# Kernel tuning notes

Measured on AMD Instinct MI355X. Metric: run time of the kernel, lower is better.

The kernel has to match this reference:

```python
import jax, jax.numpy as jnp
import numpy as np

B, H, S, D = 4, 16, 2048, 64

def setup_inputs() -> dict:
    key = jax.random.key(0)
    kq, kk, kv = jax.random.split(key, 3)
    q = jax.random.normal(kq, (B, H, S, D), dtype=jnp.float32)
    k = jax.random.normal(kk, (B, H, S, D), dtype=jnp.float32)
    v = jax.random.normal(kv, (B, H, S, D), dtype=jnp.float32)
    return {"q_tensor": q, "k_tensor": k, "v_tensor": v}

def reference(q_tensor, k_tensor, v_tensor):
    # scores: [B, H, S, S]
    inv_scale = 1.0 / jnp.sqrt(jnp.float32(k_tensor.shape[-1]))
    scores = jnp.einsum('bhqd,bhkd->bhqk', q_tensor, k_tensor) * inv_scale
    attn = jax.nn.softmax(scores, axis=-1)
    # dropout p=0.0 -> identity
    out = jnp.einsum('bhqk,bhkd->bhqd', attn, v_tensor)
    return out
```

## Files before the change

### kernel.cpp

```cpp
#include <hip/hip_runtime.h>
#include <hip/hip_bf16.h>

#define S_LEN 2048
#define D_DIM 64
#define BH 64
#define NWARP 4
#define QW 32
#define QBLK (NWARP * QW)
#define KVBLK 64
#define NKT (S_LEN / KVBLK)
#define NWG (BH * S_LEN / QBLK)
#define TILE_ELEMS (KVBLK * D_DIM)
#define TILE_BYTES (TILE_ELEMS * 2)

typedef __bf16 bf16_t;
typedef bf16_t bf16x8 __attribute__((ext_vector_type(8)));
typedef float f32x4 __attribute__((ext_vector_type(4)));
typedef float f32x16 __attribute__((ext_vector_type(16)));

typedef const __attribute__((address_space(1))) void gvoid_t;
typedef __attribute__((address_space(3))) void lvoid_t;

__device__ __forceinline__ int swz64(int row, int col) {
  return (row << 6) + (col ^ ((row & 7) << 3));
}

union W4 { unsigned u[4]; bf16x8 v; };
union PK { bf16_t h[2]; unsigned u; };

__global__ __launch_bounds__(256)
void preconv(const float* __restrict__ K, const float* __restrict__ V,
             bf16_t* __restrict__ Kws, bf16_t* __restrict__ Vws) {
  const int tile = blockIdx.x;
  const int bh = tile >> 5, kt = tile & 31;
  const size_t base = (size_t)bh * S_LEN * D_DIM + (size_t)kt * KVBLK * D_DIM;
  const int tid = threadIdx.x;
  bf16_t* ko = Kws + (size_t)tile * TILE_ELEMS;
  bf16_t* vo = Vws + (size_t)tile * TILE_ELEMS;

  const int krow = tid >> 2, kcb = tid & 3;
  const float* ks = K + base + (size_t)krow * D_DIM + kcb * 16;
  f32x4 kr[4];
#pragma unroll
  for (int i = 0; i < 4; ++i) kr[i] = *(const f32x4*)(ks + i * 4);
#pragma unroll
  for (int half = 0; half < 2; ++half) {
    bf16x8 f;
#pragma unroll
    for (int j = 0; j < 4; ++j) {
      f[j]     = (bf16_t)kr[half * 2][j];
      f[4 + j] = (bf16_t)kr[half * 2 + 1][j];
    }
    *(bf16x8*)&ko[swz64(krow, kcb * 16 + half * 8)] = f;
  }

  const int vkp = tid & 31, vdb = tid >> 5;
  const int vk0 = vkp * 2;
  const int vcol = (((vk0 >> 2) ^ (vk0 >> 3)) & 1) ? (vk0 ^ 12) : vk0;
  const float* vs = V + base + (size_t)vk0 * D_DIM + vdb * 8;
  f32x4 vr[4];
  vr[0] = *(const f32x4*)vs;           vr[1] = *(const f32x4*)(vs + 4);
  vr[2] = *(const f32x4*)(vs + D_DIM); vr[3] = *(const f32x4*)(vs + D_DIM + 4);
#pragma unroll
  for (int j = 0; j < 8; ++j) {
    PK p;
    p.h[0] = (bf16_t)((j < 4) ? vr[0][j] : vr[1][j - 4]);
    p.h[1] = (bf16_t)((j < 4) ? vr[2][j] : vr[3][j - 4]);
    *(unsigned*)&vo[swz64(vdb * 8 + j, vcol)] = p.u;
  }
}

__global__ __launch_bounds__(256, 3)
void sdpa_fwd_ws(const float* __restrict__ Q, const bf16_t* __restrict__ Kws,
                 const bf16_t* __restrict__ Vws, float* __restrict__ O) {
  __shared__ bf16_t Klds[2][TILE_ELEMS];
  __shared__ bf16_t VTlds[2][TILE_ELEMS];

  const int bid = blockIdx.x;
  const int lb  = (bid & 7) * (NWG / 8) + (bid >> 3);
  const int bx  = lb & 15;
  const int bh  = lb >> 4;

  const int tid  = threadIdx.x;
  const int wave = tid >> 6;
  const int lane = tid & 63;
  const int lq   = lane & 31;
  const int h    = lane >> 5;

  const size_t base = (size_t)bh * S_LEN * D_DIM;
  const int q0 = bx * QBLK + wave * QW;
  const float qscale = 0.125f * 1.44269504089f;

  bf16x8 qf[4];
  {
    const float* qp = Q + base + (size_t)(q0 + lq) * D_DIM + h * 8;
#pragma unroll
    for (int c = 0; c < 4; ++c) {
      f32x4 a = *(const f32x4*)(qp + c * 16);
      f32x4 b = *(const f32x4*)(qp + c * 16 + 4);
      bf16x8 f;
#pragma unroll
      for (int j = 0; j < 4; ++j) {
        f[j]     = (bf16_t)(a[j] * qscale);
        f[4 + j] = (bf16_t)(b[j] * qscale);
      }
      qf[c] = f;
    }
  }

  bf16x8 ones;
#pragma unroll
  for (int j = 0; j < 8; ++j) ones[j] = (bf16_t)1.0f;

  const char* kg = (const char*)(Kws + (size_t)(bh * NKT) * TILE_ELEMS)
                   + wave * 2048 + lane * 16;
  const char* vg = (const char*)(Vws + (size_t)(bh * NKT) * TILE_ELEMS)
                   + wave * 2048 + lane * 16;

  auto issue = [&](int kt, int buf) {
    const char* ksrc = kg + (size_t)kt * TILE_BYTES;
    const char* vsrc = vg + (size_t)kt * TILE_BYTES;
    char* kd = (char*)&Klds[buf][0] + wave * 2048;
    char* vd = (char*)&VTlds[buf][0] + wave * 2048;
    __builtin_amdgcn_global_load_lds((gvoid_t*)ksrc,          (lvoid_t*)kd,          16, 0, 0);
    __builtin_amdgcn_global_load_lds((gvoid_t*)(ksrc + 1024), (lvoid_t*)(kd + 1024), 16, 0, 0);
    __builtin_amdgcn_global_load_lds((gvoid_t*)vsrc,          (lvoid_t*)vd,          16, 0, 0);
    __builtin_amdgcn_global_load_lds((gvoid_t*)(vsrc + 1024), (lvoid_t*)(vd + 1024), 16, 0, 0);
  };

  f32x16 acc0 = {}, acc1 = {};
  f32x16 accl = {};

  issue(0, 0);

  int cur = 0;
  for (int kt = 0; kt < NKT; ++kt) {
    __builtin_amdgcn_s_barrier();
    if (kt + 1 < NKT) {
      issue(kt + 1, cur ^ 1);
      asm volatile("s_waitcnt vmcnt(4)" ::: "memory");
    } else {
      asm volatile("s_waitcnt vmcnt(0)" ::: "memory");
    }
    __builtin_amdgcn_s_barrier();
    __builtin_amdgcn_sched_barrier(0);

    const bf16_t* Kb = Klds[cur];
    const bf16_t* Vb = VTlds[cur];

    f32x16 st0 = {}, st1 = {};
    __builtin_amdgcn_s_setprio(1);
#pragma unroll
    for (int c = 0; c < 4; ++c) {
      bf16x8 kf0 = *(const bf16x8*)&Kb[swz64(lq, c * 16 + h * 8)];
      bf16x8 kf1 = *(const bf16x8*)&Kb[swz64(32 + lq, c * 16 + h * 8)];
      st0 = __builtin_amdgcn_mfma_f32_32x32x16_bf16(kf0, qf[c], st0, 0, 0, 0);
      st1 = __builtin_amdgcn_mfma_f32_32x32x16_bf16(kf1, qf[c], st1, 0, 0, 0);
    }
    __builtin_amdgcn_s_setprio(0);

#pragma unroll
    for (int r = 0; r < 16; ++r) {
      st0[r] = exp2f(st0[r]);
      st1[r] = exp2f(st1[r]);
    }

    bf16x8 pf[4];
#pragma unroll
    for (int s2 = 0; s2 < 2; ++s2) {
      W4 w0, w1;
#pragma unroll
      for (int i = 0; i < 4; ++i) {
        PK a, b;
        a.h[0] = (bf16_t)(s2 ? st1[2 * i]     : st0[2 * i]);
        a.h[1] = (bf16_t)(s2 ? st1[2 * i + 1] : st0[2 * i + 1]);
        b.h[0] = (bf16_t)(s2 ? st1[8 + 2 * i]     : st0[8 + 2 * i]);
        b.h[1] = (bf16_t)(s2 ? st1[8 + 2 * i + 1] : st0[8 + 2 * i + 1]);
        w0.u[i] = a.u; w1.u[i] = b.u;
      }
      pf[s2 * 2] = w0.v; pf[s2 * 2 + 1] = w1.v;
    }

    __builtin_amdgcn_s_setprio(1);
#pragma unroll
    for (int kc = 0; kc < 4; ++kc) {
      bf16x8 vf0 = *(const bf16x8*)&Vb[swz64(lq, kc * 16 + h * 8)];
      bf16x8 vf1 = *(const bf16x8*)&Vb[swz64(32 + lq, kc * 16 + h * 8)];
      acc0 = __builtin_amdgcn_mfma_f32_32x32x16_bf16(vf0, pf[kc], acc0, 0, 0, 0);
      acc1 = __builtin_amdgcn_mfma_f32_32x32x16_bf16(vf1, pf[kc], acc1, 0, 0, 0);
      accl = __builtin_amdgcn_mfma_f32_32x32x16_bf16(ones, pf[kc], accl, 0, 0, 0);
    }
    __builtin_amdgcn_s_setprio(0);

    cur ^= 1;
  }

  float invl = 1.0f / accl[0];
  float* op = O + base + (size_t)(q0 + lq) * D_DIM;
#pragma unroll
  for (int r = 0; r < 16; ++r) {
    int d = (r & 3) + 8 * (r >> 2) + 4 * h;
    op[d]      = acc0[r] * invl;
    op[32 + d] = acc1[r] * invl;
  }
}

__global__ __launch_bounds__(256, 2)
void sdpa_fwd_fb(const float* __restrict__ Q, const float* __restrict__ K,
                 const float* __restrict__ V, float* __restrict__ O) {
  __shared__ bf16_t Klds[2][KVBLK * D_DIM];
  __shared__ bf16_t VTlds[2][D_DIM * KVBLK];

  const int bid = blockIdx.x;
  const int lb  = (bid & 7) * (NWG / 8) + (bid >> 3);
  const int bx  = lb & 15;
  const int bh  = lb >> 4;

  const int tid  = threadIdx.x;
  const int wave = tid >> 6;
  const int lane = tid & 63;
  const int lq   = lane & 31;
  const int h    = lane >> 5;

  const size_t base = (size_t)bh * S_LEN * D_DIM;
  const int q0 = bx * QBLK + wave * QW;
  const float qscale = 0.125f * 1.44269504089f;

  bf16x8 qf[4];
  {
    const float* qp = Q + base + (size_t)(q0 + lq) * D_DIM + h * 8;
#pragma unroll
    for (int c = 0; c < 4; ++c) {
      f32x4 a = *(const f32x4*)(qp + c * 16);
      f32x4 b = *(const f32x4*)(qp + c * 16 + 4);
      bf16x8 f;
#pragma unroll
      for (int j = 0; j < 4; ++j) {
        f[j]     = (bf16_t)(a[j] * qscale);
        f[4 + j] = (bf16_t)(b[j] * qscale);
      }
      qf[c] = f;
    }
  }

  const int krow = tid >> 2, kcb = tid & 3;
  const int vkp = tid & 31, vdb = tid >> 5;
  const int vk0 = vkp * 2;
  const int vcol = (((vk0 >> 2) ^ (vk0 >> 3)) & 1) ? (vk0 ^ 12) : vk0;

  f32x4 kr[4], vr[4];

  auto issue = [&](int kt) {
    const float* ks = K + base + (size_t)(kt * KVBLK + krow) * D_DIM + kcb * 16;
#pragma unroll
    for (int i = 0; i < 4; ++i) kr[i] = *(const f32x4*)(ks + i * 4);
    const float* vs = V + base + (size_t)(kt * KVBLK + vk0) * D_DIM + vdb * 8;
    vr[0] = *(const f32x4*)vs;           vr[1] = *(const f32x4*)(vs + 4);
    vr[2] = *(const f32x4*)(vs + D_DIM); vr[3] = *(const f32x4*)(vs + D_DIM + 4);
  };

  auto stage = [&](int buf) {
#pragma unroll
    for (int half = 0; half < 2; ++half) {
      bf16x8 f;
#pragma unroll
      for (int j = 0; j < 4; ++j) {
        f[j]     = (bf16_t)kr[half * 2][j];
        f[4 + j] = (bf16_t)kr[half * 2 + 1][j];
      }
      *(bf16x8*)&Klds[buf][swz64(krow, kcb * 16 + half * 8)] = f;
    }
#pragma unroll
    for (int j = 0; j < 8; ++j) {
      PK p;
      p.h[0] = (bf16_t)((j < 4) ? vr[0][j] : vr[1][j - 4]);
      p.h[1] = (bf16_t)((j < 4) ? vr[2][j] : vr[3][j - 4]);
      *(unsigned*)&VTlds[buf][swz64(vdb * 8 + j, vcol)] = p.u;
    }
  };

  f32x16 acc0 = {}, acc1 = {};
  float m = -1e30f, l = 0.f;

  issue(0);
  stage(0);
  __syncthreads();

  for (int kt = 0; kt < NKT; ++kt) {
    const int cur = kt & 1;
    if (kt + 1 < NKT) issue(kt + 1);

    const bf16_t* Kb = Klds[cur];
    const bf16_t* Vb = VTlds[cur];

    f32x16 st0 = {}, st1 = {};
    __builtin_amdgcn_s_setprio(1);
#pragma unroll
    for (int c = 0; c < 4; ++c) {
      bf16x8 kf0 = *(const bf16x8*)&Kb[swz64(lq, c * 16 + h * 8)];
      bf16x8 kf1 = *(const bf16x8*)&Kb[swz64(32 + lq, c * 16 + h * 8)];
      st0 = __builtin_amdgcn_mfma_f32_32x32x16_bf16(kf0, qf[c], st0, 0, 0, 0);
      st1 = __builtin_amdgcn_mfma_f32_32x32x16_bf16(kf1, qf[c], st1, 0, 0, 0);
    }
    __builtin_amdgcn_s_setprio(0);

    float t16[16];
#pragma unroll
    for (int r = 0; r < 16; ++r) t16[r] = fmaxf(st0[r], st1[r]);
#pragma unroll
    for (int off = 8; off > 0; off >>= 1)
#pragma unroll
      for (int i = 0; i < off; ++i) t16[i] = fmaxf(t16[i], t16[i + off]);
    float pmax = fmaxf(t16[0], __shfl_xor(t16[0], 32, 64));

    if (!__all(pmax - m <= 8.0f)) {
      float mn = fmaxf(m, pmax);
      float al = exp2f(m - mn);
      m = mn; l *= al;
#pragma unroll
      for (int r = 0; r < 16; ++r) { acc0[r] *= al; acc1[r] *= al; }
    }

#pragma unroll
    for (int r = 0; r < 16; ++r) {
      st0[r] = exp2f(st0[r] - m);
      st1[r] = exp2f(st1[r] - m);
    }
    float sm[16];
#pragma unroll
    for (int r = 0; r < 16; ++r) sm[r] = st0[r] + st1[r];
#pragma unroll
    for (int off = 8; off > 0; off >>= 1)
#pragma unroll
      for (int i = 0; i < off; ++i) sm[i] += sm[i + off];
    l += sm[0] + __shfl_xor(sm[0], 32, 64);

    bf16x8 pf[4];
#pragma unroll
    for (int s2 = 0; s2 < 2; ++s2) {
      W4 w0, w1;
#pragma unroll
      for (int i = 0; i < 4; ++i) {
        PK a, b;
        a.h[0] = (bf16_t)(s2 ? st1[2 * i]     : st0[2 * i]);
        a.h[1] = (bf16_t)(s2 ? st1[2 * i + 1] : st0[2 * i + 1]);
        b.h[0] = (bf16_t)(s2 ? st1[8 + 2 * i]     : st0[8 + 2 * i]);
        b.h[1] = (bf16_t)(s2 ? st1[8 + 2 * i + 1] : st0[8 + 2 * i + 1]);
        w0.u[i] = a.u; w1.u[i] = b.u;
      }
      pf[s2 * 2] = w0.v; pf[s2 * 2 + 1] = w1.v;
    }

    __builtin_amdgcn_s_setprio(1);
#pragma unroll
    for (int kc = 0; kc < 4; ++kc) {
      bf16x8 vf0 = *(const bf16x8*)&Vb[swz64(lq, kc * 16 + h * 8)];
      bf16x8 vf1 = *(const bf16x8*)&Vb[swz64(32 + lq, kc * 16 + h * 8)];
      acc0 = __builtin_amdgcn_mfma_f32_32x32x16_bf16(vf0, pf[kc], acc0, 0, 0, 0);
      acc1 = __builtin_amdgcn_mfma_f32_32x32x16_bf16(vf1, pf[kc], acc1, 0, 0, 0);
    }
    __builtin_amdgcn_s_setprio(0);

    if (kt + 1 < NKT) stage(cur ^ 1);
    __syncthreads();
  }

  float invl = 1.0f / l;
  float* op = O + base + (size_t)(q0 + lq) * D_DIM;
#pragma unroll
  for (int r = 0; r < 16; ++r) {
    int d = (r & 3) + 8 * (r >> 2) + 4 * h;
    op[d]      = acc0[r] * invl;
    op[32 + d] = acc1[r] * invl;
  }
}

extern "C" void kernel_launch(void* const* d_in, const int* in_sizes, int n_in,
                              void* d_out, int out_size, void* d_ws, size_t ws_size,
                              hipStream_t stream) {
  const float* q = (const float*)d_in[0];
  const float* k = (const float*)d_in[1];
  const float* v = (const float*)d_in[2];
  float* o = (float*)d_out;

  const size_t tile_cnt = (size_t)BH * NKT;
  const size_t need = 2 * tile_cnt * TILE_ELEMS * sizeof(bf16_t);

  if (ws_size >= need) {
    bf16_t* kws = (bf16_t*)d_ws;
    bf16_t* vws = kws + tile_cnt * TILE_ELEMS;
    preconv<<<(int)tile_cnt, 256, 0, stream>>>(k, v, kws, vws);
    sdpa_fwd_ws<<<NWG, 256, 0, stream>>>(q, kws, vws, o);
  } else {
    sdpa_fwd_fb<<<NWG, 256, 0, stream>>>(q, k, v, o);
  }
}
```

Measured before the change: 123.0 us.

## Software-pipeline QK of next tile with softmax/PV of current tile

Restructures the main fast-path loop so each tile's QK^T MFMAs are issued before the previous tile's exp/PV stage, unrolled by two over even/odd LDS buffers with a single full wait-and-barrier per tile. The row sum is now taken with a VALU reduction plus a lane shuffle instead of an extra MFMA against a ones vector, and exp2f becomes the raw hardware builtin. This is meant to overlap matrix-core work with the exponentials and cut one MFMA per kv chunk, at the cost of more live registers and a stricter vmcnt(0) wait before each barrier.

```diff
diff --git a/kernel.cpp b/kernel.cpp
--- a/kernel.cpp
+++ b/kernel.cpp
@@ -108,10 +108,6 @@
     }
   }
 
-  bf16x8 ones;
-#pragma unroll
-  for (int j = 0; j < 8; ++j) ones[j] = (bf16_t)1.0f;
-
   const char* kg = (const char*)(Kws + (size_t)(bh * NKT) * TILE_ELEMS)
                    + wave * 2048 + lane * 16;
   const char* vg = (const char*)(Vws + (size_t)(bh * NKT) * TILE_ELEMS)
@@ -129,21 +125,188 @@
   };
 
   f32x16 acc0 = {}, acc1 = {};
-  f32x16 accl = {};
+  float l = 0.f;
+
+  auto qk = [&](const bf16_t* Kb, f32x16& s0, f32x16& s1) {
+    f32x16 z = {};
+    s0 = z; s1 = z;
+    __builtin_amdgcn_s_setprio(1);
+#pragma unroll
+    for (int c = 0; c < 4; ++c) {
+      bf16x8 kf0 = *(const bf16x8*)&Kb[swz64(lq, c * 16 + h * 8)];
+      bf16x8 kf1 = *(const bf16x8*)&Kb[swz64(32 + lq, c * 16 + h * 8)];
+      s0 = __builtin_amdgcn_mfma_f32_32x32x16_bf16(kf0, qf[c], s0, 0, 0, 0);
+      s1 = __builtin_amdgcn_mfma_f32_32x32x16_bf16(kf1, qf[c], s1, 0, 0, 0);
+    }
+    __builtin_amdgcn_s_setprio(0);
+  };
+
+  auto finish = [&](const bf16_t* Vb, f32x16& s0, f32x16& s1) {
+#pragma unroll
+    for (int r = 0; r < 16; ++r) {
+      s0[r] = __builtin_amdgcn_exp2f(s0[r]);
+      s1[r] = __builtin_amdgcn_exp2f(s1[r]);
+    }
+    float sm[16];
+#pragma unroll
+    for (int r = 0; r < 16; ++r) sm[r] = s0[r] + s1[r];
+#pragma unroll
+    for (int off = 8; off > 0; off >>= 1)
+#pragma unroll
+      for (int i = 0; i < off; ++i) sm[i] += sm[i + off];
+    l += sm[0] + __shfl_xor(sm[0], 32, 64);
+
+    bf16x8 pf[4];
+#pragma unroll
+    for (int s2 = 0; s2 < 2; ++s2) {
+      W4 w0, w1;
+#pragma unroll
+      for (int i = 0; i < 4; ++i) {
+        PK a, b;
+        a.h[0] = (bf16_t)(s2 ? s1[2 * i]     : s0[2 * i]);
+        a.h[1] = (bf16_t)(s2 ? s1[2 * i + 1] : s0[2 * i + 1]);
+        b.h[0] = (bf16_t)(s2 ? s1[8 + 2 * i]     : s0[8 + 2 * i]);
+        b.h[1] = (bf16_t)(s2 ? s1[8 + 2 * i + 1] : s0[8 + 2 * i + 1]);
+        w0.u[i] = a.u; w1.u[i] = b.u;
+      }
+      pf[s2 * 2] = w0.v; pf[s2 * 2 + 1] = w1.v;
+    }
+
+    __builtin_amdgcn_s_setprio(1);
+#pragma unroll
+    for (int kc = 0; kc < 4; ++kc) {
+      bf16x8 vf0 = *(const bf16x8*)&Vb[swz64(lq, kc * 16 + h * 8)];
+      bf16x8 vf1 = *(const bf16x8*)&Vb[swz64(32 + lq, kc * 16 + h * 8)];
+      acc0 = __builtin_amdgcn_mfma_f32_32x32x16_bf16(vf0, pf[kc], acc0, 0, 0, 0);
+      acc1 = __builtin_amdgcn_mfma_f32_32x32x16_bf16(vf1, pf[kc], acc1, 0, 0, 0);
+    }
+    __builtin_amdgcn_s_setprio(0);
+  };
+
+#define WAITBAR() do { \
+    asm volatile("s_waitcnt vmcnt(0) lgkmcnt(0)" ::: "memory"); \
+    __builtin_amdgcn_s_barrier(); \
+  } while (0)
+
+  f32x16 stE0, stE1, stO0, stO1;
 
   issue(0, 0);
-
-  int cur = 0;
+  WAITBAR();
+  issue(1, 1);
+  qk(Klds[0], stE0, stE1);
+
+#pragma unroll 1
+  for (int t = 1; t < NKT; t += 2) {
+    finish(VTlds[0], stE0, stE1);
+    WAITBAR();
+    if (t + 1 < NKT) issue(t + 1, 0);
+    qk(Klds[1], stO0, stO1);
+
+    if (t + 1 < NKT) {
+      finish(VTlds[1], stO0, stO1);
+      WAITBAR();
+      if (t + 2 < NKT) issue(t + 2, 1);
+      qk(Klds[0], stE0, stE1);
+    }
+  }
+  finish(VTlds[1], stO0, stO1);
+
+#undef WAITBAR
+
+  float invl = 1.0f / l;
+  float* op = O + base + (size_t)(q0 + lq) * D_DIM;
+#pragma unroll
+  for (int r = 0; r < 16; ++r) {
+    int d = (r & 3) + 8 * (r >> 2) + 4 * h;
+    op[d]      = acc0[r] * invl;
+    op[32 + d] = acc1[r] * invl;
+  }
+}
+
+__global__ __launch_bounds__(256, 2)
+void sdpa_fwd_fb(const float* __restrict__ Q, const float* __restrict__ K,
+                 const float* __restrict__ V, float* __restrict__ O) {
+  __shared__ bf16_t Klds[2][KVBLK * D_DIM];
+  __shared__ bf16_t VTlds[2][D_DIM * KVBLK];
+
+  const int bid = blockIdx.x;
+  const int lb  = (bid & 7) * (NWG / 8) + (bid >> 3);
+  const int bx  = lb & 15;
+  const int bh  = lb >> 4;
+
+  const int tid  = threadIdx.x;
+  const int wave = tid >> 6;
+  const int lane = tid & 63;
+  const int lq   = lane & 31;
+  const int h    = lane >> 5;
+
+  const size_t base = (size_t)bh * S_LEN * D_DIM;
+  const int q0 = bx * QBLK + wave * QW;
+  const float qscale = 0.125f * 1.44269504089f;
+
+  bf16x8 qf[4];
+  {
+    const float* qp = Q + base + (size_t)(q0 + lq) * D_DIM + h * 8;
+#pragma unroll
+    for (int c = 0; c < 4; ++c) {
+      f32x4 a = *(const f32x4*)(qp + c * 16);
+      f32x4 b = *(const f32x4*)(qp + c * 16 + 4);
+      bf16x8 f;
+#pragma unroll
+      for (int j = 0; j < 4; ++j) {
+        f[j]     = (bf16_t)(a[j] * qscale);
+        f[4 + j] = (bf16_t)(b[j] * qscale);
+      }
+      qf[c] = f;
+    }
+  }
+
+  const int krow = tid >> 2, kcb = tid & 3;
+  const int vkp = tid & 31, vdb = tid >> 5;
+  const int vk0 = vkp * 2;
+  const int vcol = (((vk0 >> 2) ^ (vk0 >> 3)) & 1) ? (vk0 ^ 12) : vk0;
+
+  f32x4 kr[4], vr[4];
+
+  auto issue = [&](int kt) {
+    const float* ks = K + base + (size_t)(kt * KVBLK + krow) * D_DIM + kcb * 16;
+#pragma unroll
+    for (int i = 0; i < 4; ++i) kr[i] = *(const f32x4*)(ks + i * 4);
+    const float* vs = V + base + (size_t)(kt * KVBLK + vk0) * D_DIM + vdb * 8;
+    vr[0] = *(const f32x4*)vs;           vr[1] = *(const f32x4*)(vs + 4);
+    vr[2] = *(const f32x4*)(vs + D_DIM); vr[3] = *(const f32x4*)(vs + D_DIM + 4);
+  };
+
+  auto stage = [&](int buf) {
+#pragma unroll
+    for (int half = 0; half < 2; ++half) {
+      bf16x8 f;
+#pragma unroll
+      for (int j = 0; j < 4; ++j) {
+        f[j]     = (bf16_t)kr[half * 2][j];
+        f[4 + j] = (bf16_t)kr[half * 2 + 1][j];
+      }
+      *(bf16x8*)&Klds[buf][swz64(krow, kcb * 16 + half * 8)] = f;
+    }
+#pragma unroll
+    for (int j = 0; j < 8; ++j) {
+      PK p;
+      p.h[0] = (bf16_t)((j < 4) ? vr[0][j] : vr[1][j - 4]);
+      p.h[1] = (bf16_t)((j < 4) ? vr[2][j] : vr[3][j - 4]);
+      *(unsigned*)&VTlds[buf][swz64(vdb * 8 + j, vcol)] = p.u;
+    }
+  };
+
+  f32x16 acc0 = {}, acc1 = {};
+  float m = -1e30f, l = 0.f;
+
+  issue(0);
+  stage(0);
+  __syncthreads();
+
   for (int kt = 0; kt < NKT; ++kt) {
-    __builtin_amdgcn_s_barrier();
-    if (kt + 1 < NKT) {
-      issue(kt + 1, cur ^ 1);
-      asm volatile("s_waitcnt vmcnt(4)" ::: "memory");
-    } else {
-      asm volatile("s_waitcnt vmcnt(0)" ::: "memory");
-    }
-    __builtin_amdgcn_s_barrier();
-    __builtin_amdgcn_sched_barrier(0);
+    const int cur = kt & 1;
+    if (kt + 1 < NKT) issue(kt + 1);
 
     const bf16_t* Kb = Klds[cur];
     const bf16_t* Vb = VTlds[cur];
@@ -159,11 +322,36 @@
     }
     __builtin_amdgcn_s_setprio(0);
 
+    float t16[16];
+#pragma unroll
+    for (int r = 0; r < 16; ++r) t16[r] = fmaxf(st0[r], st1[r]);
+#pragma unroll
+    for (int off = 8; off > 0; off >>= 1)
+#pragma unroll
+      for (int i = 0; i < off; ++i) t16[i] = fmaxf(t16[i], t16[i + off]);
+    float pmax = fmaxf(t16[0], __shfl_xor(t16[0], 32, 64));
+
+    if (!__all(pmax - m <= 8.0f)) {
+      float mn = fmaxf(m, pmax);
+      float al = exp2f(m - mn);
+      m = mn; l *= al;
+#pragma unroll
+      for (int r = 0; r < 16; ++r) { acc0[r] *= al; acc1[r] *= al; }
+    }
+
 #pragma unroll
     for (int r = 0; r < 16; ++r) {
-      st0[r] = exp2f(st0[r]);
-      st1[r] = exp2f(st1[r]);
-    }
+      st0[r] = exp2f(st0[r] - m);
+      st1[r] = exp2f(st1[r] - m);
+    }
+    float sm[16];
+#pragma unroll
+    for (int r = 0; r < 16; ++r) sm[r] = st0[r] + st1[r];
+#pragma unroll
+    for (int off = 8; off > 0; off >>= 1)
+#pragma unroll
+      for (int i = 0; i < off; ++i) sm[i] += sm[i + off];
+    l += sm[0] + __shfl_xor(sm[0], 32, 64);
 
     bf16x8 pf[4];
 #pragma unroll
@@ -188,176 +376,6 @@
       bf16x8 vf1 = *(const bf16x8*)&Vb[swz64(32 + lq, kc * 16 + h * 8)];
       acc0 = __builtin_amdgcn_mfma_f32_32x32x16_bf16(vf0, pf[kc], acc0, 0, 0, 0);
       acc1 = __builtin_amdgcn_mfma_f32_32x32x16_bf16(vf1, pf[kc], acc1, 0, 0, 0);
-      accl = __builtin_amdgcn_mfma_f32_32x32x16_bf16(ones, pf[kc], accl, 0, 0, 0);
-    }
-    __builtin_amdgcn_s_setprio(0);
-
-    cur ^= 1;
-  }
-
-  float invl = 1.0f / accl[0];
-  float* op = O + base + (size_t)(q0 + lq) * D_DIM;
-#pragma unroll
-  for (int r = 0; r < 16; ++r) {
-    int d = (r & 3) + 8 * (r >> 2) + 4 * h;
-    op[d]      = acc0[r] * invl;
-    op[32 + d] = acc1[r] * invl;
-  }
-}
-
-__global__ __launch_bounds__(256, 2)
-void sdpa_fwd_fb(const float* __restrict__ Q, const float* __restrict__ K,
-                 const float* __restrict__ V, float* __restrict__ O) {
-  __shared__ bf16_t Klds[2][KVBLK * D_DIM];
-  __shared__ bf16_t VTlds[2][D_DIM * KVBLK];
-
-  const int bid = blockIdx.x;
-  const int lb  = (bid & 7) * (NWG / 8) + (bid >> 3);
-  const int bx  = lb & 15;
-  const int bh  = lb >> 4;
-
-  const int tid  = threadIdx.x;
-  const int wave = tid >> 6;
-  const int lane = tid & 63;
-  const int lq   = lane & 31;
-  const int h    = lane >> 5;
-
-  const size_t base = (size_t)bh * S_LEN * D_DIM;
-  const int q0 = bx * QBLK + wave * QW;
-  const float qscale = 0.125f * 1.44269504089f;
-
-  bf16x8 qf[4];
-  {
-    const float* qp = Q + base + (size_t)(q0 + lq) * D_DIM + h * 8;
-#pragma unroll
-    for (int c = 0; c < 4; ++c) {
-      f32x4 a = *(const f32x4*)(qp + c * 16);
-      f32x4 b = *(const f32x4*)(qp + c * 16 + 4);
-      bf16x8 f;
-#pragma unroll
-      for (int j = 0; j < 4; ++j) {
-        f[j]     = (bf16_t)(a[j] * qscale);
-        f[4 + j] = (bf16_t)(b[j] * qscale);
-      }
-      qf[c] = f;
-    }
-  }
-
-  const int krow = tid >> 2, kcb = tid & 3;
-  const int vkp = tid & 31, vdb = tid >> 5;
-  const int vk0 = vkp * 2;
-  const int vcol = (((vk0 >> 2) ^ (vk0 >> 3)) & 1) ? (vk0 ^ 12) : vk0;
-
-  f32x4 kr[4], vr[4];
-
-  auto issue = [&](int kt) {
-    const float* ks = K + base + (size_t)(kt * KVBLK + krow) * D_DIM + kcb * 16;
-#pragma unroll
-    for (int i = 0; i < 4; ++i) kr[i] = *(const f32x4*)(ks + i * 4);
-    const float* vs = V + base + (size_t)(kt * KVBLK + vk0) * D_DIM + vdb * 8;
-    vr[0] = *(const f32x4*)vs;           vr[1] = *(const f32x4*)(vs + 4);
-    vr[2] = *(const f32x4*)(vs + D_DIM); vr[3] = *(const f32x4*)(vs + D_DIM + 4);
-  };
-
-  auto stage = [&](int buf) {
-#pragma unroll
-    for (int half = 0; half < 2; ++half) {
-      bf16x8 f;
-#pragma unroll
-      for (int j = 0; j < 4; ++j) {
-        f[j]     = (bf16_t)kr[half * 2][j];
-        f[4 + j] = (bf16_t)kr[half * 2 + 1][j];
-      }
-      *(bf16x8*)&Klds[buf][swz64(krow, kcb * 16 + half * 8)] = f;
-    }
-#pragma unroll
-    for (int j = 0; j < 8; ++j) {
-      PK p;
-      p.h[0] = (bf16_t)((j < 4) ? vr[0][j] : vr[1][j - 4]);
-      p.h[1] = (bf16_t)((j < 4) ? vr[2][j] : vr[3][j - 4]);
-      *(unsigned*)&VTlds[buf][swz64(vdb * 8 + j, vcol)] = p.u;
-    }
-  };
-
-  f32x16 acc0 = {}, acc1 = {};
-  float m = -1e30f, l = 0.f;
-
-  issue(0);
-  stage(0);
-  __syncthreads();
-
-  for (int kt = 0; kt < NKT; ++kt) {
-    const int cur = kt & 1;
-    if (kt + 1 < NKT) issue(kt + 1);
-
-    const bf16_t* Kb = Klds[cur];
-    const bf16_t* Vb = VTlds[cur];
-
-    f32x16 st0 = {}, st1 = {};
-    __builtin_amdgcn_s_setprio(1);
-#pragma unroll
-    for (int c = 0; c < 4; ++c) {
-      bf16x8 kf0 = *(const bf16x8*)&Kb[swz64(lq, c * 16 + h * 8)];
-      bf16x8 kf1 = *(const bf16x8*)&Kb[swz64(32 + lq, c * 16 + h * 8)];
-      st0 = __builtin_amdgcn_mfma_f32_32x32x16_bf16(kf0, qf[c], st0, 0, 0, 0);
-      st1 = __builtin_amdgcn_mfma_f32_32x32x16_bf16(kf1, qf[c], st1, 0, 0, 0);
-    }
-    __builtin_amdgcn_s_setprio(0);
-
-    float t16[16];
-#pragma unroll
-    for (int r = 0; r < 16; ++r) t16[r] = fmaxf(st0[r], st1[r]);
-#pragma unroll
-    for (int off = 8; off > 0; off >>= 1)
-#pragma unroll
-      for (int i = 0; i < off; ++i) t16[i] = fmaxf(t16[i], t16[i + off]);
-    float pmax = fmaxf(t16[0], __shfl_xor(t16[0], 32, 64));
-
-    if (!__all(pmax - m <= 8.0f)) {
-      float mn = fmaxf(m, pmax);
-      float al = exp2f(m - mn);
-      m = mn; l *= al;
-#pragma unroll
-      for (int r = 0; r < 16; ++r) { acc0[r] *= al; acc1[r] *= al; }
-    }
-
-#pragma unroll
-    for (int r = 0; r < 16; ++r) {
-      st0[r] = exp2f(st0[r] - m);
-      st1[r] = exp2f(st1[r] - m);
-    }
-    float sm[16];
-#pragma unroll
-    for (int r = 0; r < 16; ++r) sm[r] = st0[r] + st1[r];
-#pragma unroll
-    for (int off = 8; off > 0; off >>= 1)
-#pragma unroll
-      for (int i = 0; i < off; ++i) sm[i] += sm[i + off];
-    l += sm[0] + __shfl_xor(sm[0], 32, 64);
-
-    bf16x8 pf[4];
-#pragma unroll
-    for (int s2 = 0; s2 < 2; ++s2) {
-      W4 w0, w1;
-#pragma unroll
-      for (int i = 0; i < 4; ++i) {
-        PK a, b;
-        a.h[0] = (bf16_t)(s2 ? st1[2 * i]     : st0[2 * i]);
-        a.h[1] = (bf16_t)(s2 ? st1[2 * i + 1] : st0[2 * i + 1]);
-        b.h[0] = (bf16_t)(s2 ? st1[8 + 2 * i]     : st0[8 + 2 * i]);
-        b.h[1] = (bf16_t)(s2 ? st1[8 + 2 * i + 1] : st0[8 + 2 * i + 1]);
-        w0.u[i] = a.u; w1.u[i] = b.u;
-      }
-      pf[s2 * 2] = w0.v; pf[s2 * 2 + 1] = w1.v;
-    }
-
-    __builtin_amdgcn_s_setprio(1);
-#pragma unroll
-    for (int kc = 0; kc < 4; ++kc) {
-      bf16x8 vf0 = *(const bf16x8*)&Vb[swz64(lq, kc * 16 + h * 8)];
-      bf16x8 vf1 = *(const bf16x8*)&Vb[swz64(32 + lq, kc * 16 + h * 8)];
-      acc0 = __builtin_amdgcn_mfma_f32_32x32x16_bf16(vf0, pf[kc], acc0, 0, 0, 0);
-      acc1 = __builtin_amdgcn_mfma_f32_32x32x16_bf16(vf1, pf[kc], acc1, 0, 0, 0);
     }
     __builtin_amdgcn_s_setprio(0);
 
```

Result: faster. 100.6 us (-18.2%).
